# Optimization experiments

Hardware: AMD Instinct MI355X
Metric: run time of the kernel (lower is better)

Reference implementation:

```python
import jax, jax.numpy as jnp
import numpy as np

N_NODES = 50000
N_EDGES = 1600000
D = 128
N_GRAPHS = 64


def gcn_conv(x, row, col, deg_inv_sqrt, W, b):
    # GCNConv: out_i = sum_{j->i} norm_ij * (x_j @ W) + norm_ii * (x_i @ W) + b
    # with self-loops folded in and norm_ij = d_i^{-1/2} d_j^{-1/2}
    h = x @ W  # [N, H]
    norm = deg_inv_sqrt[row] * deg_inv_sqrt[col]  # [E]
    msg = h[row] * norm[:, None]  # gather over source nodes
    agg = jax.ops.segment_sum(msg, col, num_segments=N_NODES)
    agg = agg + h * (deg_inv_sqrt * deg_inv_sqrt)[:, None]  # self-loop term
    return agg + b


def setup_inputs() -> dict:
    key = jax.random.key(0)
    ks = jax.random.split(key, 12)
    x = jax.random.normal(ks[0], (N_NODES, D), dtype=jnp.float32)
    edge_index = jax.random.randint(ks[1], (2, N_EDGES), 0, N_NODES, dtype=jnp.int32)
    batch = jnp.sort(jax.random.randint(ks[2], (N_NODES,), 0, N_GRAPHS, dtype=jnp.int32))
    s = 1.0 / np.sqrt(D)
    W1 = jax.random.uniform(ks[3], (D, D), jnp.float32, -s, s)
    b1 = jax.random.uniform(ks[4], (D,), jnp.float32, -s, s)
    W2 = jax.random.uniform(ks[5], (D, D), jnp.float32, -s, s)
    b2 = jax.random.uniform(ks[6], (D,), jnp.float32, -s, s)
    W3 = jax.random.uniform(ks[7], (D, D), jnp.float32, -s, s)
    b3 = jax.random.uniform(ks[8], (D,), jnp.float32, -s, s)
    Wf = jax.random.uniform(ks[9], (D, 1), jnp.float32, -s, s)
    bf = jax.random.uniform(ks[10], (1,), jnp.float32, -s, s)
    return {"x": x, "edge_index": edge_index, "batch": batch,
            "W1": W1, "b1": b1, "W2": W2, "b2": b2, "W3": W3, "b3": b3,
            "Wf": Wf, "bf": bf}


def reference(x, edge_index, batch, W1, b1, W2, b2, W3, b3, Wf, bf):
    row, col = edge_index[0], edge_index[1]  # source -> target
    ones = jnp.ones((N_EDGES,), dtype=jnp.float32)
    deg = jax.ops.segment_sum(ones, col, num_segments=N_NODES) + 1.0  # +1 self-loop
    deg_inv_sqrt = jax.lax.rsqrt(deg)

    h = x
    for W, b in ((W1, b1), (W2, b2), (W3, b3)):
        h = gcn_conv(h, row, col, deg_inv_sqrt, W, b)
        h = jax.nn.relu(h)  # dropout is identity in eval mode (p=0)

    # global mean pool over graphs
    sums = jax.ops.segment_sum(h, batch, num_segments=N_GRAPHS)
    counts = jax.ops.segment_sum(jnp.ones((N_NODES,), jnp.float32), batch, num_segments=N_GRAPHS)
    pooled = sums / jnp.maximum(counts, 1.0)[:, None]  # [G, D]

    out = pooled @ Wf + bf  # [G, 1]
    return jax.nn.sigmoid(out)
```

## Files before the change

### kernel.cpp

```cpp
#include <hip/hip_runtime.h>
#include <hip/hip_fp16.h>
#include <math.h>

#define N_NODES 50000
#define N_EDGES 1600000
#define DIM     128
#define N_GRAPHS 64

typedef unsigned int uint32;
typedef __attribute__((ext_vector_type(8))) short bf16x8;
typedef __attribute__((ext_vector_type(4))) float f32x4;

static __device__ __forceinline__ ushort f2b(float f) {
    uint32 u = __float_as_uint(f);
    uint32 r = (u + 0x7fffu + ((u >> 16) & 1u)) >> 16;
    return (ushort)r;
}
static __device__ __forceinline__ float b2f(ushort h) {
    return __uint_as_float(((uint32)h) << 16);
}
static __device__ __forceinline__ unsigned char f2e5(float f) {
    ushort hb = __half_as_ushort(__float2half(f));
    return (unsigned char)(((uint32)hb + 0x7fu + ((hb >> 8) & 1u)) >> 8);
}
union h2u_t { uint32 u; __half2 h; };
static __device__ __forceinline__ __half2 u2h2(uint32 u) { h2u_t t; t.u = u; return t.h; }
static __device__ __forceinline__ uint32 h2u(__half2 h)  { h2u_t t; t.h = h; return t.u; }
static __device__ __forceinline__ __half2 dec01(uint32 v) {
    return u2h2(__builtin_amdgcn_perm(v, 0u, 0x05000400u));
}
static __device__ __forceinline__ __half2 dec23(uint32 v) {
    return u2h2(__builtin_amdgcn_perm(v, 0u, 0x07000600u));
}

#define NBUK 196
#define CAP  16384
#define PB1  400
#define CHUNK1 (N_EDGES / PB1)

__global__ __launch_bounds__(256) void prep_k(const float* __restrict__ W1,
                                              const float* __restrict__ W2,
                                              const float* __restrict__ W3,
                                              ushort* __restrict__ wt,
                                              int* __restrict__ gfill) {
    int blk = blockIdx.x;
    if (blk < 192) {
        int w = blk >> 6;
        const float* W = (w == 0) ? W1 : (w == 1) ? W2 : W3;
        ushort* o = wt + w * (DIM * DIM);
        int t = (blk & 63) * 256 + threadIdx.x;
        int n = t >> 7, k = t & 127;
        o[n * 128 + k] = f2b(W[k * 128 + n]);
    } else {
        int t = threadIdx.x;
        if (t < NBUK) gfill[t] = t * CAP;
    }
}

__global__ __launch_bounds__(256) void bin_k(const int* __restrict__ col,
                                             const int* __restrict__ row,
                                             int* __restrict__ gfill,
                                             uint32* __restrict__ packed) {
    __shared__ int hist[NBUK];
    __shared__ int cur[NBUK];
    int tid = threadIdx.x;
    for (int t = tid; t < NBUK; t += 256) hist[t] = 0;
    __syncthreads();
    int start = blockIdx.x * CHUNK1, end = start + CHUNK1;
    for (int e = start + tid; e < end; e += 256)
        atomicAdd(&hist[col[e] >> 8], 1);
    __syncthreads();
    for (int t = tid; t < NBUK; t += 256) {
        int h = hist[t];
        cur[t] = h ? atomicAdd(&gfill[t], h) : 0;
    }
    __syncthreads();
    for (int e = start + tid; e < end; e += 256) {
        int c = col[e];
        int r = row[e];
        int pos = atomicAdd(&cur[c >> 8], 1);
        packed[pos] = ((uint32)(c & 255) << 16) | (uint32)r;
    }
}

__global__ __launch_bounds__(256) void bucket_k(const uint32* __restrict__ packed,
                                                const int* __restrict__ gfill,
                                                int* __restrict__ cnt,
                                                int* __restrict__ offs,
                                                float* __restrict__ dis,
                                                ushort* __restrict__ csr) {
    __shared__ int bsm[256];
    __shared__ int hist[256];
    __shared__ int sm[256];
    __shared__ int lo[256];
    __shared__ int rank[256];
    int b = blockIdx.x, tid = threadIdx.x;

    int bsz = (tid < NBUK) ? (gfill[tid] - tid * CAP) : 0;
    bsm[tid] = bsz;
    __syncthreads();
    for (int off = 1; off < 256; off <<= 1) {
        int u = 0;
        if (tid >= off) u = bsm[tid - off];
        __syncthreads();
        if (tid >= off) bsm[tid] += u;
        __syncthreads();
    }
    int size = gfill[b] - b * CAP;
    int gb = bsm[b] - size;

    const uint32* pk = packed + (size_t)b * CAP;
    hist[tid] = 0; rank[tid] = 0;
    __syncthreads();
    for (int e = tid; e < size; e += 256) atomicAdd(&hist[pk[e] >> 16], 1);
    __syncthreads();
    int h = hist[tid];
    sm[tid] = h;
    __syncthreads();
    for (int off = 1; off < 256; off <<= 1) {
        int u = 0;
        if (tid >= off) u = sm[tid - off];
        __syncthreads();
        if (tid >= off) sm[tid] += u;
        __syncthreads();
    }
    lo[tid] = sm[tid] - h;
    int node = (b << 8) + tid;
    if (node < N_NODES) {
        cnt[node]  = h;
        offs[node] = gb + lo[tid];
        dis[node]  = rsqrtf((float)h + 1.0f);
    }
    __syncthreads();
    for (int e = tid; e < size; e += 256) {
        uint32 p = pk[e];
        int cl = p >> 16;
        int r = atomicAdd(&rank[cl], 1);
        csr[gb + lo[cl] + r] = (ushort)(p & 0xffffu);
    }
}

__global__ __launch_bounds__(256) void conv_k(const float* __restrict__ x, ushort* __restrict__ xb) {
    int i = blockIdx.x * blockDim.x + threadIdx.x;
    const int n4 = N_NODES * DIM / 4;
    if (i >= n4) return;
    float4 v = ((const float4*)x)[i];
    ushort4 o;
    o.x = f2b(v.x); o.y = f2b(v.y); o.z = f2b(v.z); o.w = f2b(v.w);
    ((ushort4*)xb)[i] = o;
}

__global__ __launch_bounds__(256) void gemm_mfma_k(const ushort* __restrict__ xb,
                                                   const ushort* __restrict__ wt,
                                                   const float* __restrict__ dis,
                                                   unsigned char* __restrict__ gb) {
    int wid  = threadIdx.x >> 6;
    int lane = threadIdx.x & 63;
    int r0 = blockIdx.x * 128 + wid * 32;
    int m  = lane & 15;
    int kg = lane >> 4;

    int arow0 = r0 + m;
    int arow1 = r0 + 16 + m;
    if (arow0 >= N_NODES) arow0 = N_NODES - 1;
    if (arow1 >= N_NODES) arow1 = N_NODES - 1;
    const ushort* abase0 = xb + (size_t)arow0 * DIM + kg * 8;
    const ushort* abase1 = xb + (size_t)arow1 * DIM + kg * 8;
    const ushort* wbase  = wt + (size_t)m * DIM + kg * 8;

    f32x4 acc[2][8];
    #pragma unroll
    for (int hh = 0; hh < 2; ++hh)
        #pragma unroll
        for (int nt = 0; nt < 8; ++nt) acc[hh][nt] = (f32x4){0.f, 0.f, 0.f, 0.f};

    #pragma unroll
    for (int kb = 0; kb < 4; ++kb) {
        bf16x8 a0 = *(const bf16x8*)(abase0 + kb * 32);
        bf16x8 a1 = *(const bf16x8*)(abase1 + kb * 32);
        #pragma unroll
        for (int nt = 0; nt < 8; ++nt) {
            bf16x8 b = *(const bf16x8*)(wbase + (size_t)nt * 16 * DIM + kb * 32);
            acc[0][nt] = __builtin_amdgcn_mfma_f32_16x16x32_bf16(a0, b, acc[0][nt], 0, 0, 0);
            acc[1][nt] = __builtin_amdgcn_mfma_f32_16x16x32_bf16(a1, b, acc[1][nt], 0, 0, 0);
        }
    }

    #pragma unroll
    for (int hh = 0; hh < 2; ++hh) {
        int orow0 = r0 + hh * 16 + kg * 4;
        #pragma unroll
        for (int i = 0; i < 4; ++i) {
            int rr = orow0 + i;
            if (rr >= N_NODES) continue;
            float dsc = dis[rr];
            unsigned char* orow = gb + (size_t)rr * DIM + m;
            #pragma unroll
            for (int nt = 0; nt < 8; ++nt)
                orow[nt * 16] = f2e5(acc[hh][nt][i] * dsc);
        }
    }
}

__global__ __launch_bounds__(256) void agg_k(const unsigned char* __restrict__ gb,
                                             const float* __restrict__ dis,
                                             const ushort* __restrict__ csr,
                                             const int* __restrict__ offs,
                                             const int* __restrict__ cnt,
                                             const float* __restrict__ bias,
                                             ushort* __restrict__ outb) {
    int lane = threadIdx.x & 63;
    int node = blockIdx.x * 4 + (threadIdx.x >> 6);
    if (node >= N_NODES) return;
    int hi = lane >> 5;
    uint32 c4 = (uint32)(lane & 31) << 2;
    const unsigned char* gq = gb + c4;

    uint32 sv = *(const uint32*)(gq + ((uint32)node << 7));
    if (hi) sv = 0;
    __half2 a0 = dec01(sv), b0 = dec23(sv);
    __half2 a1 = u2h2(0),   b1 = u2h2(0);

    int base = offs[node];
    int c = cnt[node];
    for (int s0 = 0; s0 < c; s0 += 64) {
        int rem = c - s0;
        int m = rem < 64 ? rem : 64;
        int idx = 0;
        if (lane < m) idx = csr[base + s0 + lane];
        int t = 0;
        for (; t + 16 <= m; t += 16) {
            uint32 v[8];
            #pragma unroll
            for (int p = 0; p < 8; ++p) {
                int j0 = __shfl(idx, t + 2 * p, 64);
                int j1 = __shfl(idx, t + 2 * p + 1, 64);
                int jr = hi ? j1 : j0;
                v[p] = *(const uint32*)(gq + ((uint32)jr << 7));
            }
            #pragma unroll
            for (int p = 0; p < 8; ++p) {
                if (p & 1) { a1 = __hadd2(a1, dec01(v[p])); b1 = __hadd2(b1, dec23(v[p])); }
                else       { a0 = __hadd2(a0, dec01(v[p])); b0 = __hadd2(b0, dec23(v[p])); }
            }
        }
        for (; t + 2 <= m; t += 2) {
            int j0 = __shfl(idx, t, 64);
            int j1 = __shfl(idx, t + 1, 64);
            int jr = hi ? j1 : j0;
            uint32 v = *(const uint32*)(gq + ((uint32)jr << 7));
            a0 = __hadd2(a0, dec01(v)); b0 = __hadd2(b0, dec23(v));
        }
        if (t < m) {
            int j = __shfl(idx, t, 64);
            uint32 v = *(const uint32*)(gq + ((uint32)j << 7));
            if (hi) v = 0;
            a0 = __hadd2(a0, dec01(v)); b0 = __hadd2(b0, dec23(v));
        }
    }

    __half2 accA = __hadd2(a0, a1);
    __half2 accB = __hadd2(b0, b1);
    accA = __hadd2(accA, u2h2((uint32)__shfl_xor((int)h2u(accA), 32, 64)));
    accB = __hadd2(accB, u2h2((uint32)__shfl_xor((int)h2u(accB), 32, 64)));

    if (hi == 0) {
        float f0 = __low2float(accA), f1 = __high2float(accA);
        float f2 = __low2float(accB), f3 = __high2float(accB);
        float d = dis[node];
        float4 bv = ((const float4*)bias)[lane & 31];
        ushort4 o;
        o.x = f2b(fmaxf(fmaf(f0, d, bv.x), 0.f));
        o.y = f2b(fmaxf(fmaf(f1, d, bv.y), 0.f));
        o.z = f2b(fmaxf(fmaf(f2, d, bv.z), 0.f));
        o.w = f2b(fmaxf(fmaf(f3, d, bv.w), 0.f));
        *(ushort4*)(outb + ((size_t)node << 7) + c4) = o;
    }
}

#define POOL_BLOCKS 512
__global__ __launch_bounds__(128) void pool_k(const ushort* __restrict__ hb,
                                              const int* __restrict__ batch,
                                              float* __restrict__ pooled,
                                              float* __restrict__ counts) {
    const int chunk = (N_NODES + POOL_BLOCKS - 1) / POOL_BLOCKS;
    int tid = threadIdx.x;
    int start = blockIdx.x * chunk;
    int end = start + chunk; if (end > N_NODES) end = N_NODES;
    if (start >= end) return;

    float acc = 0.f;
    int cur = batch[start];
    int cl = 0;
    for (int n = start; n < end; ++n) {
        int b = batch[n];
        if (b != cur) {
            atomicAdd(&pooled[cur * DIM + tid], acc);
            if (tid == 0) atomicAdd(&counts[cur], (float)cl);
            acc = 0.f; cl = 0; cur = b;
        }
        acc += b2f(hb[((size_t)n << 7) + tid]);
        ++cl;
    }
    atomicAdd(&pooled[cur * DIM + tid], acc);
    if (tid == 0) atomicAdd(&counts[cur], (float)cl);
}

__global__ void final_k(const float* __restrict__ pooled, const float* __restrict__ counts,
                        const float* __restrict__ Wf, const float* __restrict__ bf,
                        float* __restrict__ out) {
    __shared__ float sred[2];
    int gidx = blockIdx.x;
    int tid = threadIdx.x;
    float c = fmaxf(counts[gidx], 1.0f);
    float v = pooled[gidx * DIM + tid] / c * Wf[tid];
    for (int off = 32; off > 0; off >>= 1) v += __shfl_down(v, off, 64);
    if ((tid & 63) == 0) sred[tid >> 6] = v;
    __syncthreads();
    if (tid == 0) {
        float t = sred[0] + sred[1] + bf[0];
        out[gidx] = 1.0f / (1.0f + expf(-t));
    }
}

extern "C" void kernel_launch(void* const* d_in, const int* in_sizes, int n_in,
                              void* d_out, int out_size, void* d_ws, size_t ws_size,
                              hipStream_t stream) {
    const float* x     = (const float*)d_in[0];
    const int*   ei    = (const int*)d_in[1];
    const int*   batch = (const int*)d_in[2];
    const float* W1 = (const float*)d_in[3];  const float* b1 = (const float*)d_in[4];
    const float* W2 = (const float*)d_in[5];  const float* b2 = (const float*)d_in[6];
    const float* W3 = (const float*)d_in[7];  const float* b3 = (const float*)d_in[8];
    const float* Wf = (const float*)d_in[9];  const float* bf = (const float*)d_in[10];
    const int* rowp = ei;
    const int* colp = ei + N_EDGES;

    char* ws = (char*)d_ws;
    size_t o = 0;
    auto alloc = [&](size_t bytes) -> void* {
        void* p = ws + o;
        o += (bytes + 255) & ~(size_t)255;
        return p;
    };
    int*    cnt    = (int*)   alloc((size_t)N_NODES * 4);
    int*    offs   = (int*)   alloc((size_t)N_NODES * 4);
    int*    gfill  = (int*)   alloc(256 * 4);
    float*  dis    = (float*) alloc((size_t)N_NODES * 4);
    ushort* csr    = (ushort*)alloc((size_t)N_EDGES * 2);
    uint32* packed = (uint32*)alloc((size_t)NBUK * CAP * 4);
    float*  pooled = (float*) alloc((size_t)(N_GRAPHS * DIM + N_GRAPHS) * 4);
    ushort* wt     = (ushort*)alloc((size_t)3 * DIM * DIM * 2);
    unsigned char* bufA = (unsigned char*)alloc((size_t)N_NODES * DIM);
    ushort* bufB   = (ushort*)alloc((size_t)N_NODES * DIM * 2);
    float*  counts = pooled + N_GRAPHS * DIM;

    hipMemsetAsync(pooled, 0, (size_t)(N_GRAPHS * DIM + N_GRAPHS) * 4, stream);

    prep_k<<<193, 256, 0, stream>>>(W1, W2, W3, wt, gfill);
    bin_k<<<PB1, 256, 0, stream>>>(colp, rowp, gfill, packed);
    bucket_k<<<NBUK, 256, 0, stream>>>(packed, gfill, cnt, offs, dis, csr);

    conv_k<<<(N_NODES * DIM / 4 + 255) / 256, 256, 0, stream>>>(x, bufB);

    const int GB = (N_NODES + 127) / 128;

    gemm_mfma_k<<<GB, 256, 0, stream>>>(bufB, wt, dis, bufA);
    agg_k<<<(N_NODES + 3) / 4, 256, 0, stream>>>(bufA, dis, csr, offs, cnt, b1, bufB);
    gemm_mfma_k<<<GB, 256, 0, stream>>>(bufB, wt + DIM * DIM, dis, bufA);
    agg_k<<<(N_NODES + 3) / 4, 256, 0, stream>>>(bufA, dis, csr, offs, cnt, b2, bufB);
    gemm_mfma_k<<<GB, 256, 0, stream>>>(bufB, wt + 2 * DIM * DIM, dis, bufA);
    agg_k<<<(N_NODES + 3) / 4, 256, 0, stream>>>(bufA, dis, csr, offs, cnt, b3, bufB);

    pool_k<<<POOL_BLOCKS, 128, 0, stream>>>(bufB, batch, pooled, counts);
    final_k<<<N_GRAPHS, 128, 0, stream>>>(pooled, counts, Wf, bf, (float*)d_out);
}
```

Before: 253.2 us.

## Permute feature order so GEMM epilogue writes packed 8-byte fp8 rows

```diff
diff --git a/kernel.cpp b/kernel.cpp
--- a/kernel.cpp
+++ b/kernel.cpp
@@ -32,6 +32,7 @@
 static __device__ __forceinline__ __half2 dec23(uint32 v) {
     return u2h2(__builtin_amdgcn_perm(v, 0u, 0x07000600u));
 }
+static __device__ __forceinline__ int permf(int p) { return ((p & 7) << 4) + (p >> 3); }
 
 #define NBUK 196
 #define CAP  16384
@@ -49,8 +50,9 @@
         const float* W = (w == 0) ? W1 : (w == 1) ? W2 : W3;
         ushort* o = wt + w * (DIM * DIM);
         int t = (blk & 63) * 256 + threadIdx.x;
-        int n = t >> 7, k = t & 127;
-        o[n * 128 + k] = f2b(W[k * 128 + n]);
+        int n = t >> 7, kp = t & 127;
+        int f = (w == 0) ? kp : permf(kp);
+        o[n * 128 + kp] = f2b(W[f * 128 + n]);
     } else {
         int t = threadIdx.x;
         if (t < NBUK) gfill[t] = t * CAP;
@@ -194,10 +196,16 @@
             int rr = orow0 + i;
             if (rr >= N_NODES) continue;
             float dsc = dis[rr];
-            unsigned char* orow = gb + (size_t)rr * DIM + m;
-            #pragma unroll
-            for (int nt = 0; nt < 8; ++nt)
-                orow[nt * 16] = f2e5(acc[hh][nt][i] * dsc);
+            uint32 u0 = (uint32)f2e5(acc[hh][0][i] * dsc)
+                      | ((uint32)f2e5(acc[hh][1][i] * dsc) << 8)
+                      | ((uint32)f2e5(acc[hh][2][i] * dsc) << 16)
+                      | ((uint32)f2e5(acc[hh][3][i] * dsc) << 24);
+            uint32 u1 = (uint32)f2e5(acc[hh][4][i] * dsc)
+                      | ((uint32)f2e5(acc[hh][5][i] * dsc) << 8)
+                      | ((uint32)f2e5(acc[hh][6][i] * dsc) << 16)
+                      | ((uint32)f2e5(acc[hh][7][i] * dsc) << 24);
+            uint2 u = make_uint2(u0, u1);
+            *(uint2*)(gb + (size_t)rr * DIM + m * 8) = u;
         }
     }
 }
@@ -268,17 +276,20 @@
         float f0 = __low2float(accA), f1 = __high2float(accA);
         float f2 = __low2float(accB), f3 = __high2float(accB);
         float d = dis[node];
-        float4 bv = ((const float4*)bias)[lane & 31];
+        float bv0 = bias[permf(c4 + 0)];
+        float bv1 = bias[permf(c4 + 1)];
+        float bv2 = bias[permf(c4 + 2)];
+        float bv3 = bias[permf(c4 + 3)];
         ushort4 o;
-        o.x = f2b(fmaxf(fmaf(f0, d, bv.x), 0.f));
-        o.y = f2b(fmaxf(fmaf(f1, d, bv.y), 0.f));
-        o.z = f2b(fmaxf(fmaf(f2, d, bv.z), 0.f));
-        o.w = f2b(fmaxf(fmaf(f3, d, bv.w), 0.f));
+        o.x = f2b(fmaxf(fmaf(f0, d, bv0), 0.f));
+        o.y = f2b(fmaxf(fmaf(f1, d, bv1), 0.f));
+        o.z = f2b(fmaxf(fmaf(f2, d, bv2), 0.f));
+        o.w = f2b(fmaxf(fmaf(f3, d, bv3), 0.f));
         *(ushort4*)(outb + ((size_t)node << 7) + c4) = o;
     }
 }
 
-#define POOL_BLOCKS 512
+#define POOL_BLOCKS 1024
 __global__ __launch_bounds__(128) void pool_k(const ushort* __restrict__ hb,
                                               const int* __restrict__ batch,
                                               float* __restrict__ pooled,
@@ -313,7 +324,7 @@
     int gidx = blockIdx.x;
     int tid = threadIdx.x;
     float c = fmaxf(counts[gidx], 1.0f);
-    float v = pooled[gidx * DIM + tid] / c * Wf[tid];
+    float v = pooled[gidx * DIM + tid] / c * Wf[permf(tid)];
     for (int off = 32; off > 0; off >>= 1) v += __shfl_down(v, off, 64);
     if ((tid & 63) == 0) sred[tid >> 6] = v;
     __syncthreads();
```

Result: faster. 241.1 us (-4.8%).
